# Performance work log

Hardware: AMD Instinct MI355X
Metric: run time of the kernel (lower is better)

The kernel has to match this reference:

```python
import jax, jax.numpy as jnp
import numpy as np

NEG_SLOPE = 0.2  # PyG GATConv default leaky_relu slope
EPS = 1e-16     # PyG softmax denominator epsilon


def gat_conv(x, src, dst, edge_attr, W, att_src, att_dst, W_edge, att_edge, bias):
    """Single-head PyG GATConv with edge_dim. x:[N,Fin] -> [N,Fout].
    src/dst already include self-loops; edge_attr matches their length."""
    N = x.shape[0]
    h = x @ W                      # [N, Fout] transformed node features
    a_s = h @ att_src              # [N] per-node source logit contribution
    a_d = h @ att_dst              # [N]
    a_e = (edge_attr @ W_edge) @ att_edge   # [E] edge contribution
    logits = jax.nn.leaky_relu(a_s[src] + a_d[dst] + a_e, NEG_SLOPE)  # [E]
    # segment softmax over destination nodes
    m = jax.ops.segment_max(logits, dst, num_segments=N)    # [N]
    m = jnp.where(jnp.isfinite(m), m, 0.0)
    e = jnp.exp(logits - m[dst])                             # [E]
    denom = jax.ops.segment_sum(e, dst, num_segments=N)      # [N]
    alpha = e / (denom[dst] + EPS)                            # [E]
    # scatter-aggregate weighted messages
    out = jax.ops.segment_sum(alpha[:, None] * h[src], dst, num_segments=N)
    return out + bias


def setup_inputs() -> dict:
    key = jax.random.key(0)
    ks = jax.random.split(key, 16)
    N, E, F_in, H, C, ED = 100000, 1600000, 128, 64, 2, 1
    inp = {
        "x": jax.random.normal(ks[0], (N, F_in), dtype=jnp.float32),
        "edge_index": jax.random.randint(ks[1], (2, E), 0, N, dtype=jnp.int32),
        "edge_attr": jax.random.normal(ks[2], (E, ED), dtype=jnp.float32),
        # layer 1 params (Glorot-ish scale)
        "W1": jax.random.normal(ks[3], (F_in, H), dtype=jnp.float32) * (1.0 / np.sqrt(F_in)),
        "att_src1": jax.random.normal(ks[4], (H,), dtype=jnp.float32) * (1.0 / np.sqrt(H)),
        "att_dst1": jax.random.normal(ks[5], (H,), dtype=jnp.float32) * (1.0 / np.sqrt(H)),
        "W_edge1": jax.random.normal(ks[6], (ED, H), dtype=jnp.float32),
        "att_edge1": jax.random.normal(ks[7], (H,), dtype=jnp.float32) * (1.0 / np.sqrt(H)),
        "bias1": jnp.zeros((H,), dtype=jnp.float32),
        # layer 2 params
        "W2": jax.random.normal(ks[8], (H, C), dtype=jnp.float32) * (1.0 / np.sqrt(H)),
        "att_src2": jax.random.normal(ks[9], (C,), dtype=jnp.float32),
        "att_dst2": jax.random.normal(ks[10], (C,), dtype=jnp.float32),
        "W_edge2": jax.random.normal(ks[11], (ED, C), dtype=jnp.float32),
        "att_edge2": jax.random.normal(ks[12], (C,), dtype=jnp.float32),
        "bias2": jnp.zeros((C,), dtype=jnp.float32),
    }
    return inp


def reference(x, edge_index, edge_attr,
              W1, att_src1, att_dst1, W_edge1, att_edge1, bias1,
              W2, att_src2, att_dst2, W_edge2, att_edge2, bias2):
    N = x.shape[0]
    # PyG GATConv add_self_loops=True, fill_value='mean' for edge_attr
    loop = jnp.arange(N, dtype=edge_index.dtype)
    src = jnp.concatenate([edge_index[0], loop])
    dst = jnp.concatenate([edge_index[1], loop])
    ea_mean = jnp.mean(edge_attr, axis=0, keepdims=True)              # [1, ED]
    ea = jnp.concatenate([edge_attr, jnp.broadcast_to(ea_mean, (N, edge_attr.shape[1]))])

    h = gat_conv(x, src, dst, ea, W1, att_src1, att_dst1, W_edge1, att_edge1, bias1)
    h = jax.nn.relu(h)  # dropout is identity in eval mode
    out = gat_conv(h, src, dst, ea, W2, att_src2, att_dst2, W_edge2, att_edge2, bias2)
    return jax.nn.log_softmax(out, axis=1)
```

## Files before the change

kernel.cpp:

```cpp
#include <hip/hip_runtime.h>
#include <math.h>

#define NEG_SLOPE 0.2f
#define EPSF 1e-16f

constexpr int FIN = 128;
constexpr int H   = 64;
constexpr int C   = 2;
constexpr int BSHIFT = 8;
constexpr int NBUCK_MAX = 1024;
constexpr int CHUNK = 4096;
constexpr int CAP   = 6144;

typedef short v8s __attribute__((ext_vector_type(8)));
typedef float v4f __attribute__((ext_vector_type(4)));
typedef unsigned short u16;

__device__ inline void split_bf16(float v, u16& hi, u16& lo) {
    unsigned u = __float_as_uint(v);
    unsigned r = (u + 0x7FFFu + ((u >> 16) & 1u)) >> 16;
    hi = (u16)r;
    float hf = __uint_as_float(r << 16);
    float l = v - hf;
    unsigned ul = __float_as_uint(l);
    lo = (u16)((ul + 0x7FFFu + ((ul >> 16) & 1u)) >> 16);
}

__device__ inline u16 to_bf16(float v) {
    unsigned u = __float_as_uint(v);
    return (u16)((u + 0x7FFFu + ((u >> 16) & 1u)) >> 16);
}
__device__ inline float blo(int v) { return __uint_as_float((unsigned)v << 16); }
__device__ inline float bhi(int v) { return __uint_as_float((unsigned)v & 0xFFFF0000u); }

__global__ __launch_bounds__(256) void pre_kernel(const float* __restrict__ ea,
                                                  const int* __restrict__ dst, int E,
                                                  float* __restrict__ sum_ea, int* __restrict__ cnt,
                                                  const float* __restrict__ W1,
                                                  u16* __restrict__ Wt_hi, u16* __restrict__ Wt_lo,
                                                  int NBUCK) {
    int c = blockIdx.x, t = threadIdx.x;
    int gid = c * 256 + t;
    if (gid < FIN * H) {
        int k = gid >> 6, f = gid & 63;
        u16 h, l;
        split_bf16(W1[gid], h, l);
        int idx = ((k >> 3) << 9) + (f << 3) + (k & 7);
        Wt_hi[idx] = h;
        Wt_lo[idx] = l;
    }
    __shared__ int lh[NBUCK_MAX];
    for (int i = t; i < NBUCK_MAX; i += 256) lh[i] = 0;
    __syncthreads();
    int base = c * CHUNK;
    int cntE = min(CHUNK, E - base);
    float acc = 0.f;
    for (int i = t; i < cntE; i += 256) {
        int e = base + i;
        acc += ea[e];
        atomicAdd(&lh[dst[e] >> BSHIFT], 1);
    }
    for (int off = 32; off; off >>= 1) acc += __shfl_down(acc, off, 64);
    __shared__ float wsum[4];
    int lane = t & 63, wv = t >> 6;
    if (lane == 0) wsum[wv] = acc;
    __syncthreads();
    if (t == 0) atomicAdd(sum_ea, wsum[0] + wsum[1] + wsum[2] + wsum[3]);
    for (int i = t; i < NBUCK; i += 256)
        cnt[(size_t)c * NBUCK + i] = lh[i];
}

__global__ __launch_bounds__(256) void soff_kernel(const int* __restrict__ cnt,
                                                   int NBUCK, int NCHUNK,
                                                   int* __restrict__ bcount, int* __restrict__ poff) {
    int b = blockIdx.x, t = threadIdx.x;
    int per = (NCHUNK + 255) / 256;
    int v[8];
    int s = 0;
    for (int j = 0; j < per; j++) {
        int c = t * per + j;
        v[j] = (c < NCHUNK) ? cnt[(size_t)c * NBUCK + b] : 0;
        s += v[j];
    }
    __shared__ int red[256];
    red[t] = s;
    __syncthreads();
    for (int off = 1; off < 256; off <<= 1) {
        int u = (t >= off) ? red[t - off] : 0;
        __syncthreads();
        red[t] += u;
        __syncthreads();
    }
    int run = red[t] - s;
    for (int j = 0; j < per; j++) {
        int c = t * per + j;
        if (c < NCHUNK) poff[(size_t)b * NCHUNK + c] = run;
        run += v[j];
    }
    if (t == 255) bcount[b] = red[255];
}

__global__ __launch_bounds__(1024) void bscan_kernel(const int* __restrict__ bcount, int NBUCK, int E,
                                                     int* __restrict__ bbase,
                                                     int* __restrict__ rowN,
                                                     const float* __restrict__ sum_ea,
                                                     const float* __restrict__ W_edge1,
                                                     const float* __restrict__ att_edge1,
                                                     const float* __restrict__ W_edge2,
                                                     const float* __restrict__ att_edge2,
                                                     float* __restrict__ scal) {
    int t = threadIdx.x;
    if (t == 0) {
        float m = *sum_ea / (float)E;
        float c1 = 0.f;
        for (int i = 0; i < H; i++) c1 += W_edge1[i] * att_edge1[i];
        float c2 = 0.f;
        for (int i = 0; i < C; i++) c2 += W_edge2[i] * att_edge2[i];
        scal[0] = m; scal[1] = c1; scal[2] = c2;
    }
    __shared__ int sh[1024];
    int v = (t < NBUCK) ? bcount[t] : 0;
    sh[t] = v;
    __syncthreads();
    for (int off = 1; off < 1024; off <<= 1) {
        int u = (t >= off) ? sh[t - off] : 0;
        __syncthreads();
        sh[t] += u;
        __syncthreads();
    }
    if (t < NBUCK) bbase[t] = sh[t] - v;
    if (t == 0) { bbase[NBUCK] = E; *rowN = E; }
}

__global__ __launch_bounds__(256) void stage_kernel(
        const int* __restrict__ src, const int* __restrict__ dst, const float* __restrict__ ea,
        int E, const int* __restrict__ cnt, const int* __restrict__ poff,
        const int* __restrict__ bbase,
        int2* __restrict__ staging, int NBUCK, int NCHUNK) {
    __shared__ int   cur[NBUCK_MAX];
    __shared__ int   gofs[NBUCK_MAX];
    __shared__ int2  sbuf[CHUNK];
    __shared__ short sbkt[CHUNK];
    __shared__ int   red[256];
    int t = threadIdx.x;
    int c = blockIdx.x;
    int base = c * CHUNK;
    int cntE = min(CHUNK, E - base);
    int i0 = t * 4;
    int h[4];
    #pragma unroll
    for (int j = 0; j < 4; j++) {
        int i = i0 + j;
        h[j] = (i < NBUCK) ? cnt[(size_t)c * NBUCK + i] : 0;
    }
    int s = h[0] + h[1] + h[2] + h[3];
    red[t] = s;
    __syncthreads();
    for (int off = 1; off < 256; off <<= 1) {
        int u = (t >= off) ? red[t - off] : 0;
        __syncthreads();
        red[t] += u;
        __syncthreads();
    }
    int p = red[t] - s;
    #pragma unroll
    for (int j = 0; j < 4; j++) {
        int i = i0 + j;
        if (i < NBUCK) {
            if (h[j]) gofs[i] = bbase[i] + poff[(size_t)i * NCHUNK + c] - p;
            cur[i] = p;
        }
        p += h[j];
    }
    __syncthreads();
    for (int i = t; i < cntE; i += 256) {
        int e = base + i;
        int d = dst[e];
        int b = d >> BSHIFT;
        int slot = atomicAdd(&cur[b], 1);
        sbuf[slot] = make_int2(src[e] | ((d & ((1 << BSHIFT) - 1)) << 20), __float_as_int(ea[e]));
        sbkt[slot] = (short)b;
    }
    __syncthreads();
    for (int j = t; j < cntE; j += 256)
        staging[gofs[sbkt[j]] + j] = sbuf[j];
}

__global__ __launch_bounds__(256) void gemm1_mfma_kernel(
        const float* __restrict__ x,
        const u16* __restrict__ Wt_hi, const u16* __restrict__ Wt_lo,
        const float* __restrict__ att_src, const float* __restrict__ att_dst,
        u16* __restrict__ h1b, float* __restrict__ a_s, float* __restrict__ a_d, int N) {
    __shared__ u16 WhL[FIN * H];
    __shared__ u16 WlL[FIN * H];
    int t = threadIdx.x;
    int w = t >> 6, lane = t & 63;
    int m = lane & 15, q = lane >> 4;
    int base = blockIdx.x * 64 + w * 16;
    int nodeA = base + m;
    bool inA = nodeA < N;
    const float* xrow = x + (size_t)nodeA * FIN;

    float4 fh[4], fl4[4];
    {
        const float4* gh = (const float4*)Wt_hi;
        const float4* gl = (const float4*)Wt_lo;
        #pragma unroll
        for (int i = 0; i < 4; i++) {
            fh[i]  = gh[t + i * 256];
            fl4[i] = gl[t + i * 256];
        }
    }
    float4 xv4[8];
    #pragma unroll
    for (int kt = 0; kt < 4; kt++) {
        if (inA) {
            const float4* p = (const float4*)(xrow + kt * 32 + q * 8);
            xv4[kt * 2]     = p[0];
            xv4[kt * 2 + 1] = p[1];
        } else {
            xv4[kt * 2]     = make_float4(0.f, 0.f, 0.f, 0.f);
            xv4[kt * 2 + 1] = make_float4(0.f, 0.f, 0.f, 0.f);
        }
    }
    {
        float4* sh = (float4*)WhL;
        float4* sl = (float4*)WlL;
        #pragma unroll
        for (int i = 0; i < 4; i++) {
            sh[t + i * 256] = fh[i];
            sl[t + i * 256] = fl4[i];
        }
    }

    v8s ah[4], al[4];
    #pragma unroll
    for (int kt = 0; kt < 4; kt++) {
        float xv[8];
        xv[0] = xv4[kt * 2].x;     xv[1] = xv4[kt * 2].y;
        xv[2] = xv4[kt * 2].z;     xv[3] = xv4[kt * 2].w;
        xv[4] = xv4[kt * 2 + 1].x; xv[5] = xv4[kt * 2 + 1].y;
        xv[6] = xv4[kt * 2 + 1].z; xv[7] = xv4[kt * 2 + 1].w;
        #pragma unroll
        for (int j = 0; j < 8; j++) {
            u16 hb, lb;
            split_bf16(xv[j], hb, lb);
            ah[kt][j] = (short)hb;
            al[kt][j] = (short)lb;
        }
    }
    __syncthreads();

    float ps[4] = {0.f, 0.f, 0.f, 0.f};
    float pd[4] = {0.f, 0.f, 0.f, 0.f};
    #pragma unroll
    for (int ft = 0; ft < 4; ft++) {
        v4f acc = {0.f, 0.f, 0.f, 0.f};
        #pragma unroll
        for (int kt = 0; kt < 4; kt++) {
            int fi = ((kt * 4 + q) << 9) + ((ft * 16 + m) << 3);
            v8s bh = *(const v8s*)(WhL + fi);
            v8s bl = *(const v8s*)(WlL + fi);
            acc = __builtin_amdgcn_mfma_f32_16x16x32_bf16(ah[kt], bh, acc, 0, 0, 0);
            acc = __builtin_amdgcn_mfma_f32_16x16x32_bf16(al[kt], bh, acc, 0, 0, 0);
            acc = __builtin_amdgcn_mfma_f32_16x16x32_bf16(ah[kt], bl, acc, 0, 0, 0);
        }
        int f = ft * 16 + m;
        float asf = att_src[f], adf = att_dst[f];
        #pragma unroll
        for (int r = 0; r < 4; r++) {
            int node = base + q * 4 + r;
            if (node < N) h1b[(size_t)node * H + f] = to_bf16(acc[r]);
            ps[r] += acc[r] * asf;
            pd[r] += acc[r] * adf;
        }
    }
    #pragma unroll
    for (int msk = 1; msk < 16; msk <<= 1) {
        #pragma unroll
        for (int r = 0; r < 4; r++) {
            ps[r] += __shfl_xor(ps[r], msk, 64);
            pd[r] += __shfl_xor(pd[r], msk, 64);
        }
    }
    if (m == 0) {
        #pragma unroll
        for (int r = 0; r < 4; r++) {
            int node = base + q * 4 + r;
            if (node < N) { a_s[node] = ps[r]; a_d[node] = pd[r]; }
        }
    }
}

__global__ __launch_bounds__(256) void bfin_kernel(
        const int2* __restrict__ staging, const int* __restrict__ bbase,
        const float* __restrict__ scal,
        const float* __restrict__ a_s1, const float* __restrict__ a_d1,
        int* __restrict__ row, int2* __restrict__ sedge, float* __restrict__ sea2, int N) {
    __shared__ int   nh[256];
    __shared__ int   red[256];
    __shared__ int2  ebuf[CAP];
    __shared__ float abuf[CAP];
    int b = blockIdx.x, t = threadIdx.x;
    int beg = bbase[b], end = bbase[b + 1];
    int cnt = end - beg;
    int node0 = b << BSHIFT;
    float c1 = scal[1];
    nh[t] = 0;
    __syncthreads();
    for (int i = beg + t; i < end; i += 256)
        atomicAdd(&nh[(unsigned)staging[i].x >> 20], 1);
    __syncthreads();
    int v = nh[t];
    red[t] = v;
    __syncthreads();
    for (int off = 1; off < 256; off <<= 1) {
        int u = (t >= off) ? red[t - off] : 0;
        __syncthreads();
        red[t] += u;
        __syncthreads();
    }
    int excl = red[t] - v;
    int node = node0 + t;
    if (node < N) row[node] = beg + excl;
    __syncthreads();
    bool fast = (cnt <= CAP);
    nh[t] = fast ? excl : beg + excl;
    __syncthreads();
    for (int i = beg + t; i < end; i += 256) {
        int2 r = staging[i];
        int dlow = (unsigned)r.x >> 20;
        int sn = r.x & 0xFFFFF;
        float eav = __int_as_float(r.y);
        float lg = a_s1[sn] + a_d1[node0 + dlow] + eav * c1;
        lg = lg > 0.f ? lg : NEG_SLOPE * lg;
        float ex = __expf(lg);
        int pos = atomicAdd(&nh[dlow], 1);
        if (fast) {
            ebuf[pos] = make_int2(sn, __float_as_int(ex));
            abuf[pos] = eav;
        } else {
            sedge[pos] = make_int2(sn, __float_as_int(ex));
            sea2[pos] = eav;
        }
    }
    __syncthreads();
    if (fast) {
        for (int j = t; j < cnt; j += 256) {
            sedge[beg + j] = ebuf[j];
            sea2[beg + j]  = abuf[j];
        }
    }
}

__global__ __launch_bounds__(256) void agg1_kernel(
        const int* __restrict__ row, const int2* __restrict__ sedge,
        const float* __restrict__ scal,
        const float* __restrict__ a_s, const float* __restrict__ a_d,
        const u16* __restrict__ h1b,
        const float* __restrict__ bias1, const float* __restrict__ W2,
        const float* __restrict__ att_src2, const float* __restrict__ att_dst2,
        float* __restrict__ h2, float* __restrict__ a_s2, float* __restrict__ a_d2,
        int N) {
    int wv = threadIdx.x >> 6;
    int lane = threadIdx.x & 63;
    int g  = lane >> 3;
    int fl = lane & 7;
    int n = blockIdx.x * 32 + wv * 8 + g;
    if (n >= N) return;
    int beg = row[n], end = row[n + 1];
    float den = 0.f;
    float acc[8] = {0.f, 0.f, 0.f, 0.f, 0.f, 0.f, 0.f, 0.f};
    const u16* hrow = h1b + fl * 8;
    int i = beg;
    for (; i + 2 <= end; i += 2) {
        int2 e0 = sedge[i], e1 = sedge[i + 1];
        int4 h0 = *(const int4*)(hrow + (size_t)e0.x * H);
        int4 h1v = *(const int4*)(hrow + (size_t)e1.x * H);
        float x0 = __int_as_float(e0.y), x1 = __int_as_float(e1.y);
        den += x0 + x1;
        acc[0] += x0 * blo(h0.x); acc[1] += x0 * bhi(h0.x);
        acc[2] += x0 * blo(h0.y); acc[3] += x0 * bhi(h0.y);
        acc[4] += x0 * blo(h0.z); acc[5] += x0 * bhi(h0.z);
        acc[6] += x0 * blo(h0.w); acc[7] += x0 * bhi(h0.w);
        acc[0] += x1 * blo(h1v.x); acc[1] += x1 * bhi(h1v.x);
        acc[2] += x1 * blo(h1v.y); acc[3] += x1 * bhi(h1v.y);
        acc[4] += x1 * blo(h1v.z); acc[5] += x1 * bhi(h1v.z);
        acc[6] += x1 * blo(h1v.w); acc[7] += x1 * bhi(h1v.w);
    }
    if (i < end) {
        int2 e0 = sedge[i];
        int4 h0 = *(const int4*)(hrow + (size_t)e0.x * H);
        float x0 = __int_as_float(e0.y);
        den += x0;
        acc[0] += x0 * blo(h0.x); acc[1] += x0 * bhi(h0.x);
        acc[2] += x0 * blo(h0.y); acc[3] += x0 * bhi(h0.y);
        acc[4] += x0 * blo(h0.z); acc[5] += x0 * bhi(h0.z);
        acc[6] += x0 * blo(h0.w); acc[7] += x0 * bhi(h0.w);
    }
    {
        float lg = a_s[n] + a_d[n] + scal[0] * scal[1];
        lg = lg > 0.f ? lg : NEG_SLOPE * lg;
        float ex = __expf(lg);
        int4 hs = *(const int4*)(hrow + (size_t)n * H);
        den += ex;
        acc[0] += ex * blo(hs.x); acc[1] += ex * bhi(hs.x);
        acc[2] += ex * blo(hs.y); acc[3] += ex * bhi(hs.y);
        acc[4] += ex * blo(hs.z); acc[5] += ex * bhi(hs.z);
        acc[6] += ex * blo(hs.w); acc[7] += ex * bhi(hs.w);
    }
    float inv = 1.f / (den + EPSF);
    float p0 = 0.f, p1 = 0.f;
    #pragma unroll
    for (int k = 0; k < 8; k++) {
        int f = fl * 8 + k;
        float hr = acc[k] * inv + bias1[f];
        hr = fmaxf(hr, 0.f);
        p0 += hr * W2[f * C + 0];
        p1 += hr * W2[f * C + 1];
    }
    #pragma unroll
    for (int msk = 1; msk < 8; msk <<= 1) {
        p0 += __shfl_xor(p0, msk, 64);
        p1 += __shfl_xor(p1, msk, 64);
    }
    if (fl == 0) {
        h2[(size_t)n * C + 0] = p0;
        h2[(size_t)n * C + 1] = p1;
        a_s2[n] = p0 * att_src2[0] + p1 * att_src2[1];
        a_d2[n] = p0 * att_dst2[0] + p1 * att_dst2[1];
    }
}

__global__ __launch_bounds__(256) void agg2_kernel(
        const int* __restrict__ row, const int2* __restrict__ sedge, const float* __restrict__ sea2,
        const float* __restrict__ scal,
        const float* __restrict__ a_s2, const float* __restrict__ a_d2,
        const float* __restrict__ h2, const float* __restrict__ bias2,
        float* __restrict__ out, int N) {
    int wv = threadIdx.x >> 6;
    int lane = threadIdx.x & 63;
    int g  = lane >> 3;
    int fl = lane & 7;
    int n = blockIdx.x * 32 + wv * 8 + g;
    if (n >= N) return;
    float c2 = scal[2];
    float ad = a_d2[n];
    int beg = row[n], end = row[n + 1];
    float den = 0.f, m0 = 0.f, m1 = 0.f;
    for (int i = beg + fl; i < end; i += 8) {
        int s = sedge[i].x;
        float lg = a_s2[s] + ad + sea2[i] * c2;
        lg = lg > 0.f ? lg : NEG_SLOPE * lg;
        float ex = __expf(lg);
        den += ex;
        m0 += ex * h2[(size_t)s * C + 0];
        m1 += ex * h2[(size_t)s * C + 1];
    }
    if (fl == 0) {
        float lg = a_s2[n] + ad + scal[0] * c2;
        lg = lg > 0.f ? lg : NEG_SLOPE * lg;
        float ex = __expf(lg);
        den += ex;
        m0 += ex * h2[(size_t)n * C + 0];
        m1 += ex * h2[(size_t)n * C + 1];
    }
    #pragma unroll
    for (int msk = 1; msk < 8; msk <<= 1) {
        den += __shfl_xor(den, msk, 64);
        m0  += __shfl_xor(m0, msk, 64);
        m1  += __shfl_xor(m1, msk, 64);
    }
    if (fl == 0) {
        float dn = den + EPSF;
        float o0 = m0 / dn + bias2[0];
        float o1 = m1 / dn + bias2[1];
        float mx = fmaxf(o0, o1);
        float lse = mx + logf(expf(o0 - mx) + expf(o1 - mx));
        out[(size_t)n * C + 0] = o0 - lse;
        out[(size_t)n * C + 1] = o1 - lse;
    }
}

extern "C" void kernel_launch(void* const* d_in, const int* in_sizes, int n_in,
                              void* d_out, int out_size, void* d_ws, size_t ws_size,
                              hipStream_t stream) {
    const float* x        = (const float*)d_in[0];
    const int*   ei       = (const int*)d_in[1];
    const float* ea       = (const float*)d_in[2];
    const float* W1       = (const float*)d_in[3];
    const float* att_src1 = (const float*)d_in[4];
    const float* att_dst1 = (const float*)d_in[5];
    const float* W_edge1  = (const float*)d_in[6];
    const float* att_edge1= (const float*)d_in[7];
    const float* bias1    = (const float*)d_in[8];
    const float* W2       = (const float*)d_in[9];
    const float* att_src2 = (const float*)d_in[10];
    const float* att_dst2 = (const float*)d_in[11];
    const float* W_edge2  = (const float*)d_in[12];
    const float* att_edge2= (const float*)d_in[13];
    const float* bias2    = (const float*)d_in[14];

    const int N  = in_sizes[0] / FIN;
    const int E  = in_sizes[1] / 2;
    const int* srcp = ei;
    const int* dstp = ei + E;
    const int NBUCK  = (N + (1 << BSHIFT) - 1) >> BSHIFT;
    const int NCHUNK = (E + CHUNK - 1) / CHUNK;

    char* wsb = (char*)d_ws;
    size_t off = 0;
    auto alloc = [&](size_t bytes) { void* p = wsb + off; off += (bytes + 255) & ~size_t(255); return p; };
    float* sum_ea = (float*)alloc(4);
    size_t zbytes = off;
    int*   bcount = (int*)alloc((size_t)NBUCK_MAX * 4);
    int*   bbase  = (int*)alloc((size_t)(NBUCK_MAX + 1) * 4);
    int*   cnt    = (int*)alloc((size_t)NCHUNK * NBUCK * 4);
    int*   poff   = (int*)alloc((size_t)NBUCK * NCHUNK * 4);
    int*   row    = (int*)alloc((size_t)(N + 1) * 4);
    int2*  sedge  = (int2*)alloc((size_t)(E + 8) * 8);
    float* sea2   = (float*)alloc((size_t)E * 4);
    int2*  staging= (int2*)alloc((size_t)E * 8);
    u16*   h1b    = (u16*)alloc((size_t)N * H * 2);
    u16*   Wt_hi  = (u16*)alloc((size_t)FIN * H * 2);
    u16*   Wt_lo  = (u16*)alloc((size_t)FIN * H * 2);
    float* a_s1   = (float*)alloc((size_t)N * 4);
    float* a_d1   = (float*)alloc((size_t)N * 4);
    float* h2     = (float*)alloc((size_t)N * C * 4);
    float* a_s2   = (float*)alloc((size_t)N * 4);
    float* a_d2   = (float*)alloc((size_t)N * 4);
    float* scal   = (float*)alloc(3 * 4);

    hipMemsetAsync(d_ws, 0, zbytes, stream);

    pre_kernel<<<NCHUNK, 256, 0, stream>>>(ea, dstp, E, sum_ea, cnt, W1, Wt_hi, Wt_lo, NBUCK);
    soff_kernel<<<NBUCK, 256, 0, stream>>>(cnt, NBUCK, NCHUNK, bcount, poff);
    bscan_kernel<<<1, 1024, 0, stream>>>(bcount, NBUCK, E, bbase, row + N,
                                         sum_ea, W_edge1, att_edge1, W_edge2, att_edge2, scal);
    stage_kernel<<<NCHUNK, 256, 0, stream>>>(srcp, dstp, ea, E, cnt, poff, bbase,
                                             staging, NBUCK, NCHUNK);
    gemm1_mfma_kernel<<<(N + 63) / 64, 256, 0, stream>>>(x, Wt_hi, Wt_lo, att_src1, att_dst1,
                                                         h1b, a_s1, a_d1, N);
    bfin_kernel<<<NBUCK, 256, 0, stream>>>(staging, bbase, scal, a_s1, a_d1, row, sedge, sea2, N);
    agg1_kernel<<<(N + 31) / 32, 256, 0, stream>>>(row, sedge, scal, a_s1, a_d1, h1b,
                                                   bias1, W2, att_src2, att_dst2,
                                                   h2, a_s2, a_d2, N);
    agg2_kernel<<<(N + 31) / 32, 256, 0, stream>>>(row, sedge, sea2, scal, a_s2, a_d2, h2, bias2,
                                                   (float*)d_out, N);
}
```

Baseline: 238.4 us.

## Remove memset and bucket-scan kernel; fold scans into staging, widen blocks

Removes the hipMemsetAsync and the single-block bscan kernel. Each block writes its partial edge-attr sum, and soff block 0 reduces those sums deterministically. Every stage block recomputes the bucket exclusive scan with a wave-shuffle scan (block 0 writes bbase), and pre/stage/bfin now run with 1024 threads and shuffle scans instead of LDS Hillis-Steele loops. The aim is fewer launches and serialized tiny kernels, at the cost of redundant scan work per block and lower occupancy from larger blocks with big LDS footprints.

```diff
diff --git a/kernel.cpp b/kernel.cpp
--- a/kernel.cpp
+++ b/kernel.cpp
@@ -33,14 +33,29 @@
 __device__ inline float blo(int v) { return __uint_as_float((unsigned)v << 16); }
 __device__ inline float bhi(int v) { return __uint_as_float((unsigned)v & 0xFFFF0000u); }
 
-__global__ __launch_bounds__(256) void pre_kernel(const float* __restrict__ ea,
-                                                  const int* __restrict__ dst, int E,
-                                                  float* __restrict__ sum_ea, int* __restrict__ cnt,
-                                                  const float* __restrict__ W1,
-                                                  u16* __restrict__ Wt_hi, u16* __restrict__ Wt_lo,
-                                                  int NBUCK) {
+__device__ inline int scan1024_excl(int v, int* wtot, int t) {
+    int lane = t & 63, w = t >> 6;
+    int incl = v;
+    #pragma unroll
+    for (int o = 1; o < 64; o <<= 1) {
+        int u = __shfl_up(incl, o, 64);
+        if (lane >= o) incl += u;
+    }
+    if (lane == 63) wtot[w] = incl;
+    __syncthreads();
+    int woff = 0;
+    for (int i = 0; i < w; i++) woff += wtot[i];
+    return woff + incl - v;
+}
+
+__global__ __launch_bounds__(1024) void pre_kernel(const float* __restrict__ ea,
+                                                   const int* __restrict__ dst, int E,
+                                                   float* __restrict__ csum, int* __restrict__ cnt,
+                                                   const float* __restrict__ W1,
+                                                   u16* __restrict__ Wt_hi, u16* __restrict__ Wt_lo,
+                                                   int NBUCK) {
     int c = blockIdx.x, t = threadIdx.x;
-    int gid = c * 256 + t;
+    int gid = c * 1024 + t;
     if (gid < FIN * H) {
         int k = gid >> 6, f = gid & 63;
         u16 h, l;
@@ -50,29 +65,40 @@
         Wt_lo[idx] = l;
     }
     __shared__ int lh[NBUCK_MAX];
-    for (int i = t; i < NBUCK_MAX; i += 256) lh[i] = 0;
+    __shared__ float wsum[16];
+    lh[t] = 0;
     __syncthreads();
     int base = c * CHUNK;
     int cntE = min(CHUNK, E - base);
     float acc = 0.f;
-    for (int i = t; i < cntE; i += 256) {
+    for (int i = t; i < cntE; i += 1024) {
         int e = base + i;
         acc += ea[e];
         atomicAdd(&lh[dst[e] >> BSHIFT], 1);
     }
     for (int off = 32; off; off >>= 1) acc += __shfl_down(acc, off, 64);
-    __shared__ float wsum[4];
     int lane = t & 63, wv = t >> 6;
     if (lane == 0) wsum[wv] = acc;
     __syncthreads();
-    if (t == 0) atomicAdd(sum_ea, wsum[0] + wsum[1] + wsum[2] + wsum[3]);
-    for (int i = t; i < NBUCK; i += 256)
-        cnt[(size_t)c * NBUCK + i] = lh[i];
+    if (t == 0) {
+        float s = 0.f;
+        #pragma unroll
+        for (int i = 0; i < 16; i++) s += wsum[i];
+        csum[c] = s;
+    }
+    if (t < NBUCK) cnt[(size_t)c * NBUCK + t] = lh[t];
 }
 
 __global__ __launch_bounds__(256) void soff_kernel(const int* __restrict__ cnt,
                                                    int NBUCK, int NCHUNK,
-                                                   int* __restrict__ bcount, int* __restrict__ poff) {
+                                                   int* __restrict__ bcount, int* __restrict__ poff,
+                                                   const float* __restrict__ csum, int E,
+                                                   const float* __restrict__ W_edge1,
+                                                   const float* __restrict__ att_edge1,
+                                                   const float* __restrict__ W_edge2,
+                                                   const float* __restrict__ att_edge2,
+                                                   float* __restrict__ scal,
+                                                   int* __restrict__ rowN) {
     int b = blockIdx.x, t = threadIdx.x;
     int per = (NCHUNK + 255) / 256;
     int v[8];
@@ -83,6 +109,7 @@
         s += v[j];
     }
     __shared__ int red[256];
+    __shared__ float ws4[4];
     red[t] = s;
     __syncthreads();
     for (int off = 1; off < 256; off <<= 1) {
@@ -98,82 +125,55 @@
         run += v[j];
     }
     if (t == 255) bcount[b] = red[255];
-}
-
-__global__ __launch_bounds__(1024) void bscan_kernel(const int* __restrict__ bcount, int NBUCK, int E,
-                                                     int* __restrict__ bbase,
-                                                     int* __restrict__ rowN,
-                                                     const float* __restrict__ sum_ea,
-                                                     const float* __restrict__ W_edge1,
-                                                     const float* __restrict__ att_edge1,
-                                                     const float* __restrict__ W_edge2,
-                                                     const float* __restrict__ att_edge2,
-                                                     float* __restrict__ scal) {
-    int t = threadIdx.x;
-    if (t == 0) {
-        float m = *sum_ea / (float)E;
-        float c1 = 0.f;
-        for (int i = 0; i < H; i++) c1 += W_edge1[i] * att_edge1[i];
-        float c2 = 0.f;
-        for (int i = 0; i < C; i++) c2 += W_edge2[i] * att_edge2[i];
-        scal[0] = m; scal[1] = c1; scal[2] = c2;
-    }
-    __shared__ int sh[1024];
-    int v = (t < NBUCK) ? bcount[t] : 0;
-    sh[t] = v;
-    __syncthreads();
-    for (int off = 1; off < 1024; off <<= 1) {
-        int u = (t >= off) ? sh[t - off] : 0;
+    if (b == 0) {
+        float acc = 0.f;
+        for (int i = t; i < NCHUNK; i += 256) acc += csum[i];
+        for (int off = 32; off; off >>= 1) acc += __shfl_down(acc, off, 64);
+        if ((t & 63) == 0) ws4[t >> 6] = acc;
         __syncthreads();
-        sh[t] += u;
-        __syncthreads();
-    }
-    if (t < NBUCK) bbase[t] = sh[t] - v;
-    if (t == 0) { bbase[NBUCK] = E; *rowN = E; }
-}
-
-__global__ __launch_bounds__(256) void stage_kernel(
+        if (t == 0) {
+            float tot = ws4[0] + ws4[1] + ws4[2] + ws4[3];
+            float c1 = 0.f;
+            for (int i = 0; i < H; i++) c1 += W_edge1[i] * att_edge1[i];
+            float c2 = 0.f;
+            for (int i = 0; i < C; i++) c2 += W_edge2[i] * att_edge2[i];
+            scal[0] = tot / (float)E; scal[1] = c1; scal[2] = c2;
+            *rowN = E;
+        }
+    }
+}
+
+__global__ __launch_bounds__(1024) void stage_kernel(
         const int* __restrict__ src, const int* __restrict__ dst, const float* __restrict__ ea,
         int E, const int* __restrict__ cnt, const int* __restrict__ poff,
-        const int* __restrict__ bbase,
-        int2* __restrict__ staging, int NBUCK, int NCHUNK) {
+        const int* __restrict__ bcount,
+        int2* __restrict__ staging, int* __restrict__ bbase_out, int NBUCK, int NCHUNK) {
+    __shared__ int   bb[NBUCK_MAX];
     __shared__ int   cur[NBUCK_MAX];
     __shared__ int   gofs[NBUCK_MAX];
     __shared__ int2  sbuf[CHUNK];
     __shared__ short sbkt[CHUNK];
-    __shared__ int   red[256];
+    __shared__ int   wt16[16];
     int t = threadIdx.x;
     int c = blockIdx.x;
     int base = c * CHUNK;
     int cntE = min(CHUNK, E - base);
-    int i0 = t * 4;
-    int h[4];
-    #pragma unroll
-    for (int j = 0; j < 4; j++) {
-        int i = i0 + j;
-        h[j] = (i < NBUCK) ? cnt[(size_t)c * NBUCK + i] : 0;
-    }
-    int s = h[0] + h[1] + h[2] + h[3];
-    red[t] = s;
-    __syncthreads();
-    for (int off = 1; off < 256; off <<= 1) {
-        int u = (t >= off) ? red[t - off] : 0;
-        __syncthreads();
-        red[t] += u;
-        __syncthreads();
-    }
-    int p = red[t] - s;
-    #pragma unroll
-    for (int j = 0; j < 4; j++) {
-        int i = i0 + j;
-        if (i < NBUCK) {
-            if (h[j]) gofs[i] = bbase[i] + poff[(size_t)i * NCHUNK + c] - p;
-            cur[i] = p;
-        }
-        p += h[j];
-    }
-    __syncthreads();
-    for (int i = t; i < cntE; i += 256) {
+    int bv = (t < NBUCK) ? bcount[t] : 0;
+    int bx = scan1024_excl(bv, wt16, t);
+    if (t < NBUCK) bb[t] = bx;
+    if (c == 0) {
+        if (t < NBUCK) bbase_out[t] = bx;
+        if (t == 0) bbase_out[NBUCK] = E;
+    }
+    __syncthreads();
+    int h = (t < NBUCK) ? cnt[(size_t)c * NBUCK + t] : 0;
+    int p = scan1024_excl(h, wt16, t);
+    if (t < NBUCK) {
+        if (h) gofs[t] = bb[t] + poff[(size_t)t * NCHUNK + c] - p;
+        cur[t] = p;
+    }
+    __syncthreads();
+    for (int i = t; i < cntE; i += 1024) {
         int e = base + i;
         int d = dst[e];
         int b = d >> BSHIFT;
@@ -182,7 +182,7 @@
         sbkt[slot] = (short)b;
     }
     __syncthreads();
-    for (int j = t; j < cntE; j += 256)
+    for (int j = t; j < cntE; j += 1024)
         staging[gofs[sbkt[j]] + j] = sbuf[j];
 }
 
@@ -292,13 +292,13 @@
     }
 }
 
-__global__ __launch_bounds__(256) void bfin_kernel(
+__global__ __launch_bounds__(1024) void bfin_kernel(
         const int2* __restrict__ staging, const int* __restrict__ bbase,
         const float* __restrict__ scal,
         const float* __restrict__ a_s1, const float* __restrict__ a_d1,
         int* __restrict__ row, int2* __restrict__ sedge, float* __restrict__ sea2, int N) {
     __shared__ int   nh[256];
-    __shared__ int   red[256];
+    __shared__ int   wt16[16];
     __shared__ int2  ebuf[CAP];
     __shared__ float abuf[CAP];
     int b = blockIdx.x, t = threadIdx.x;
@@ -306,28 +306,31 @@
     int cnt = end - beg;
     int node0 = b << BSHIFT;
     float c1 = scal[1];
-    nh[t] = 0;
-    __syncthreads();
-    for (int i = beg + t; i < end; i += 256)
+    if (t < 256) nh[t] = 0;
+    __syncthreads();
+    for (int i = beg + t; i < end; i += 1024)
         atomicAdd(&nh[(unsigned)staging[i].x >> 20], 1);
     __syncthreads();
-    int v = nh[t];
-    red[t] = v;
-    __syncthreads();
-    for (int off = 1; off < 256; off <<= 1) {
-        int u = (t >= off) ? red[t - off] : 0;
-        __syncthreads();
-        red[t] += u;
-        __syncthreads();
-    }
-    int excl = red[t] - v;
+    int v = (t < 256) ? nh[t] : 0;
+    int lane = t & 63, w = t >> 6;
+    int incl = v;
+    #pragma unroll
+    for (int o = 1; o < 64; o <<= 1) {
+        int u = __shfl_up(incl, o, 64);
+        if (lane >= o) incl += u;
+    }
+    if (w < 4 && lane == 63) wt16[w] = incl;
+    __syncthreads();
+    int woff = 0;
+    int wl = w < 4 ? w : 4;
+    for (int i = 0; i < wl; i++) woff += wt16[i];
+    int excl = woff + incl - v;
     int node = node0 + t;
-    if (node < N) row[node] = beg + excl;
-    __syncthreads();
+    if (t < 256 && node < N) row[node] = beg + excl;
     bool fast = (cnt <= CAP);
-    nh[t] = fast ? excl : beg + excl;
-    __syncthreads();
-    for (int i = beg + t; i < end; i += 256) {
+    if (t < 256) nh[t] = fast ? excl : beg + excl;
+    __syncthreads();
+    for (int i = beg + t; i < end; i += 1024) {
         int2 r = staging[i];
         int dlow = (unsigned)r.x >> 20;
         int sn = r.x & 0xFFFFF;
@@ -346,7 +349,7 @@
     }
     __syncthreads();
     if (fast) {
-        for (int j = t; j < cnt; j += 256) {
+        for (int j = t; j < cnt; j += 1024) {
             sedge[beg + j] = ebuf[j];
             sea2[beg + j]  = abuf[j];
         }
@@ -511,8 +514,7 @@
     char* wsb = (char*)d_ws;
     size_t off = 0;
     auto alloc = [&](size_t bytes) { void* p = wsb + off; off += (bytes + 255) & ~size_t(255); return p; };
-    float* sum_ea = (float*)alloc(4);
-    size_t zbytes = off;
+    float* csum   = (float*)alloc((size_t)2048 * 4);
     int*   bcount = (int*)alloc((size_t)NBUCK_MAX * 4);
     int*   bbase  = (int*)alloc((size_t)(NBUCK_MAX + 1) * 4);
     int*   cnt    = (int*)alloc((size_t)NCHUNK * NBUCK * 4);
@@ -531,17 +533,15 @@
     float* a_d2   = (float*)alloc((size_t)N * 4);
     float* scal   = (float*)alloc(3 * 4);
 
-    hipMemsetAsync(d_ws, 0, zbytes, stream);
-
-    pre_kernel<<<NCHUNK, 256, 0, stream>>>(ea, dstp, E, sum_ea, cnt, W1, Wt_hi, Wt_lo, NBUCK);
-    soff_kernel<<<NBUCK, 256, 0, stream>>>(cnt, NBUCK, NCHUNK, bcount, poff);
-    bscan_kernel<<<1, 1024, 0, stream>>>(bcount, NBUCK, E, bbase, row + N,
-                                         sum_ea, W_edge1, att_edge1, W_edge2, att_edge2, scal);
-    stage_kernel<<<NCHUNK, 256, 0, stream>>>(srcp, dstp, ea, E, cnt, poff, bbase,
-                                             staging, NBUCK, NCHUNK);
+    pre_kernel<<<NCHUNK, 1024, 0, stream>>>(ea, dstp, E, csum, cnt, W1, Wt_hi, Wt_lo, NBUCK);
+    soff_kernel<<<NBUCK, 256, 0, stream>>>(cnt, NBUCK, NCHUNK, bcount, poff,
+                                           csum, E, W_edge1, att_edge1, W_edge2, att_edge2,
+                                           scal, row + N);
+    stage_kernel<<<NCHUNK, 1024, 0, stream>>>(srcp, dstp, ea, E, cnt, poff, bcount,
+                                              staging, bbase, NBUCK, NCHUNK);
     gemm1_mfma_kernel<<<(N + 63) / 64, 256, 0, stream>>>(x, Wt_hi, Wt_lo, att_src1, att_dst1,
                                                          h1b, a_s1, a_d1, N);
-    bfin_kernel<<<NBUCK, 256, 0, stream>>>(staging, bbase, scal, a_s1, a_d1, row, sedge, sea2, N);
+    bfin_kernel<<<NBUCK, 1024, 0, stream>>>(staging, bbase, scal, a_s1, a_d1, row, sedge, sea2, N);
     agg1_kernel<<<(N + 31) / 32, 256, 0, stream>>>(row, sedge, scal, a_s1, a_d1, h1b,
                                                    bias1, W2, att_src2, att_dst2,
                                                    h2, a_s2, a_d2, N);
```

After: 216.4 us. 9.2% less time.
